# Performance work log

Hardware: AMD Instinct MI355X
Metric: run time of the kernel (lower is better)

## Reference

```python
import jax, jax.numpy as jnp
import numpy as np

N_NODES = 100000
N_EDGES = 800000


def setup_inputs() -> dict:
    key = jax.random.key(0)
    ks = jax.random.split(key, 9)
    def glorot(k, shape):
        lim = float(np.sqrt(6.0 / (shape[0] + shape[1])))
        return jax.random.uniform(k, shape, jnp.float32, -lim, lim)
    return {
        "x": jax.random.normal(ks[0], (N_NODES, 4), jnp.float32),
        "edge_index": jax.random.randint(ks[1], (2, N_EDGES), 0, N_NODES, jnp.int64),
        "edge_weight": jax.random.uniform(ks[2], (N_EDGES,), jnp.float32),
        "W1": glorot(ks[3], (4, 128)),
        "b1": jnp.zeros((128,), jnp.float32),
        "W2": glorot(ks[4], (128, 64)),
        "b2": jnp.zeros((64,), jnp.float32),
        "W3": glorot(ks[5], (64, 1)),
        "b3": jnp.zeros((1,), jnp.float32),
    }


def reference(x, edge_index, edge_weight, W1, b1, W2, b2, W3, b3):
    N = x.shape[0]
    # PyG GCNConv: add self loops (weight 1) and symmetric normalization.
    loop = jnp.arange(N)
    src = jnp.concatenate([edge_index[0], loop])  # [E+N]
    dst = jnp.concatenate([edge_index[1], loop])  # [E+N]
    w = jnp.concatenate([edge_weight, jnp.ones((N,), x.dtype)])
    deg = jax.ops.segment_sum(w, dst, num_segments=N)  # weighted in-degree
    dis = jnp.where(deg > 0, jax.lax.rsqrt(jnp.maximum(deg, 1e-12)), 0.0)
    norm = dis[src] * w * dis[dst]  # [E+N]

    def conv(h, W, b):
        h = h @ W                      # [N, F_out] transform first (F_out small)
        msg = norm[:, None] * h[src]   # gather + scale per edge
        return jax.ops.segment_sum(msg, dst, num_segments=N) + b

    h = jax.nn.relu(conv(x, W1, b1))
    h = jax.nn.relu(conv(h, W2, b2))
    return conv(h, W3, b3)
```

## Files before the change

### kernel.cpp

```cpp
#include <hip/hip_runtime.h>
#include <hip/hip_fp16.h>


constexpr int N = 100000;
constexpr int E = 800000;
constexpr int NBKT = 391;
constexpr int BCAP = 3072;
constexpr int GC = 125;
constexpr int CHUNK = 6400;

static inline int cdiv(int a, int b) { return (a + b - 1) / b; }

typedef __attribute__((ext_vector_type(8))) _Float16 f16x8;
typedef __attribute__((ext_vector_type(4))) float f32x4;

__global__ void k_zero(int* __restrict__ bucket_cursor) {
    int i = blockIdx.x * blockDim.x + threadIdx.x;
    if (i < NBKT) bucket_cursor[i] = 0;
}

__global__ __launch_bounds__(256) void k_coarse(const int* __restrict__ src,
                                                const int* __restrict__ dst,
                                                const float* __restrict__ w,
                                                int* __restrict__ bucket_cursor,
                                                int2* __restrict__ sorted) {
    __shared__ int hist[NBKT];
    __shared__ int base[NBKT];
    int t = threadIdx.x;
    for (int i = t; i < NBKT; i += 256) hist[i] = 0;
    __syncthreads();
    int begin = blockIdx.x * CHUNK;
    int ranks[25];
#pragma unroll
    for (int i = 0; i < 25; i++) {
        int e = begin + i * 256 + t;
        ranks[i] = atomicAdd(&hist[dst[e] >> 8], 1);
    }
    __syncthreads();
    for (int i = t; i < NBKT; i += 256) {
        int h = hist[i];
        base[i] = h ? atomicAdd(&bucket_cursor[i], h) : 0;
    }
    __syncthreads();
#pragma unroll
    for (int i = 0; i < 25; i++) {
        int e = begin + i * 256 + t;
        int d = dst[e], b = d >> 8;
        int pos = base[b] + ranks[i];
        if (pos < BCAP)
            sorted[(size_t)b * BCAP + pos] =
                make_int2(src[e] | ((d & 255) << 17), __float_as_int(w[e]));
    }
}

__global__ __launch_bounds__(256) void k_fine(const int2* __restrict__ sorted,
                                              const int* __restrict__ bucket_cursor,
                                              int cap, int2* __restrict__ payload,
                                              int* __restrict__ cursor,
                                              float* __restrict__ dis) {
    __shared__ int   ncnt[256];
    __shared__ float nwsum[256];
    int t = threadIdx.x, b = blockIdx.x;
    ncnt[t] = 0;
    nwsum[t] = 1.0f;
    __syncthreads();
    int cnt = bucket_cursor[b]; if (cnt > BCAP) cnt = BCAP;
    const int2* seg = sorted + (size_t)b * BCAP;
    for (int i = t; i < cnt; i += 256) {
        int2 r = seg[i];
        int s = r.x & 0x1FFFF, dlo = r.x >> 17;
        int pos = atomicAdd(&ncnt[dlo], 1);
        atomicAdd(&nwsum[dlo], __int_as_float(r.y));
        if (pos < cap)
            payload[(size_t)(b * 256 + dlo) * cap + pos] = make_int2(s, r.y);
    }
    __syncthreads();
    int n = b * 256 + t;
    if (n < N) {
        int c = ncnt[t]; if (c > cap) c = cap;
        cursor[n] = c;
        dis[n] = rsqrtf(nwsum[t]);
    }
}

__global__ void k_agg1(const float4* __restrict__ x, const float* __restrict__ dis,
                       const int* __restrict__ cursor, const int2* __restrict__ payload,
                       int cap, float4* __restrict__ agg1) {
    int n = blockIdx.x * blockDim.x + threadIdx.x;
    if (n >= N) return;
    float di = dis[n], sc = di * di;
    float4 v = x[n];
    float ax = sc * v.x, ay = sc * v.y, az = sc * v.z, aw = sc * v.w;
    int c = cursor[n];
    const int2* row = payload + (size_t)n * cap;
    for (int e = 0; e < c; e++) {
        int2 p = row[e];
        float nm = dis[p.x] * __int_as_float(p.y) * di;
        float4 u = x[p.x];
        ax = fmaf(nm, u.x, ax); ay = fmaf(nm, u.y, ay);
        az = fmaf(nm, u.z, az); aw = fmaf(nm, u.w, aw);
    }
    agg1[n] = make_float4(ax, ay, az, aw);
}

constexpr int HROW = 136;
__global__ __launch_bounds__(256) void k_fused_l1(const float4* __restrict__ agg1,
                                                  const float* __restrict__ W1,
                                                  const float* __restrict__ b1,
                                                  const float* __restrict__ W2,
                                                  __half* __restrict__ y2h) {
    __shared__ _Float16 h1lds[4][16 * HROW];
    int t = threadIdx.x, wave = t >> 6, lane = t & 63;
    int q = lane >> 4, c = lane & 15;
    _Float16* sh = h1lds[wave];

    int k1 = lane, k2 = lane + 64;
    float w10 = W1[0 * 128 + k1], w11 = W1[1 * 128 + k1];
    float w12 = W1[2 * 128 + k1], w13 = W1[3 * 128 + k1], bb1 = b1[k1];
    float w20 = W1[0 * 128 + k2], w21 = W1[1 * 128 + k2];
    float w22 = W1[2 * 128 + k2], w23 = W1[3 * 128 + k2], bb2 = b1[k2];

    f16x8 Bf[4][4];
#pragma unroll
    for (int kt = 0; kt < 4; kt++)
#pragma unroll
        for (int nt = 0; nt < 4; nt++)
#pragma unroll
            for (int j = 0; j < 8; j++)
                Bf[kt][nt][j] = (_Float16)W2[(kt * 32 + q * 8 + j) * 64 + nt * 16 + c];

    int wave_id = blockIdx.x * 4 + wave;
#pragma unroll
    for (int g = 0; g < 2; g++) {
        int n0 = (wave_id * 2 + g) * 16;
        if (n0 >= N) break;
#pragma unroll
        for (int m = 0; m < 16; m++) {
            float4 a = agg1[n0 + m];
            float v1 = bb1, v2 = bb2;
            v1 = fmaf(a.x, w10, v1); v1 = fmaf(a.y, w11, v1);
            v1 = fmaf(a.z, w12, v1); v1 = fmaf(a.w, w13, v1);
            v2 = fmaf(a.x, w20, v2); v2 = fmaf(a.y, w21, v2);
            v2 = fmaf(a.z, w22, v2); v2 = fmaf(a.w, w23, v2);
            sh[m * HROW + k1] = (_Float16)fmaxf(v1, 0.f);
            sh[m * HROW + k2] = (_Float16)fmaxf(v2, 0.f);
        }
        f32x4 C[4] = {{0.f, 0.f, 0.f, 0.f}, {0.f, 0.f, 0.f, 0.f},
                      {0.f, 0.f, 0.f, 0.f}, {0.f, 0.f, 0.f, 0.f}};
#pragma unroll
        for (int kt = 0; kt < 4; kt++) {
            f16x8 A = *(const f16x8*)&sh[c * HROW + kt * 32 + q * 8];
#pragma unroll
            for (int nt = 0; nt < 4; nt++)
                C[nt] = __builtin_amdgcn_mfma_f32_16x16x32_f16(A, Bf[kt][nt], C[nt], 0, 0, 0);
        }
#pragma unroll
        for (int nt = 0; nt < 4; nt++)
#pragma unroll
            for (int r = 0; r < 4; r++) {
                int node = n0 + q * 4 + r;
                y2h[(size_t)node * 64 + nt * 16 + c] = __float2half(C[nt][r]);
            }
    }
}

__global__ __launch_bounds__(256) void k_agg2_fused(
        const __half* __restrict__ y2h, const float* __restrict__ dis,
        const int* __restrict__ cursor, const int2* __restrict__ payload, int cap,
        const float* __restrict__ b2, const float* __restrict__ W3,
        const float* __restrict__ b3, float* __restrict__ s_out,
        float* __restrict__ out) {
    int t = threadIdx.x, wave = t >> 6, lane = t & 63;
    int n = blockIdx.x * 4 + wave;
    if (n >= N) return;
    float di = dis[n];
    float acc = di * di * __half2float(y2h[(size_t)n * 64 + lane]);
    int c = cursor[n];
    const int2* row = payload + (size_t)n * cap;
    int e = 0;
    for (; e + 3 < c; e += 4) {
        int2 p0 = row[e], p1 = row[e + 1], p2 = row[e + 2], p3 = row[e + 3];
        float v0 = __half2float(y2h[(size_t)p0.x * 64 + lane]);
        float v1 = __half2float(y2h[(size_t)p1.x * 64 + lane]);
        float v2 = __half2float(y2h[(size_t)p2.x * 64 + lane]);
        float v3 = __half2float(y2h[(size_t)p3.x * 64 + lane]);
        acc = fmaf(dis[p0.x] * __int_as_float(p0.y) * di, v0, acc);
        acc = fmaf(dis[p1.x] * __int_as_float(p1.y) * di, v1, acc);
        acc = fmaf(dis[p2.x] * __int_as_float(p2.y) * di, v2, acc);
        acc = fmaf(dis[p3.x] * __int_as_float(p3.y) * di, v3, acc);
    }
    for (; e < c; e++) {
        int2 p = row[e];
        acc = fmaf(dis[p.x] * __int_as_float(p.y) * di,
                   __half2float(y2h[(size_t)p.x * 64 + lane]), acc);
    }
    float h = fmaxf(acc + b2[lane], 0.f);
    float p = h * W3[lane];
#pragma unroll
    for (int off = 32; off > 0; off >>= 1) p += __shfl_down(p, off);
    if (lane == 0) {
        s_out[n] = p;
        out[n] = di * di * p + b3[0];
    }
}

__global__ void k_agg3(const float* __restrict__ s, const float* __restrict__ dis,
                       const int* __restrict__ cursor, const int2* __restrict__ payload,
                       int cap, float* __restrict__ out) {
    int n = blockIdx.x * blockDim.x + threadIdx.x;
    if (n >= N) return;
    float di = dis[n], acc = 0.f;
    int c = cursor[n];
    const int2* row = payload + (size_t)n * cap;
    for (int e = 0; e < c; e++) {
        int2 p = row[e];
        acc = fmaf(dis[p.x] * __int_as_float(p.y) * di, s[p.x], acc);
    }
    out[n] += acc;
}

extern "C" void kernel_launch(void* const* d_in, const int* in_sizes, int n_in,
                              void* d_out, int out_size, void* d_ws, size_t ws_size,
                              hipStream_t stream) {
    const float* x  = (const float*)d_in[0];
    const int*   ei = (const int*)d_in[1];
    const int* src = ei;
    const int* dst = ei + E;
    const float* w  = (const float*)d_in[2];
    const float* W1 = (const float*)d_in[3];
    const float* b1 = (const float*)d_in[4];
    const float* W2 = (const float*)d_in[5];
    const float* b2 = (const float*)d_in[6];
    const float* W3 = (const float*)d_in[7];
    const float* b3 = (const float*)d_in[8];
    float* out = (float*)d_out;

    int*    bcur    = (int*)d_ws;
    int*    cursor  = bcur + 512;
    float*  dis     = (float*)(cursor + N);
    float*  agg1    = dis + N;
    __half* y2h     = (__half*)(agg1 + 4 * N);
    float*  s       = agg1;
    int2*   sorted  = (int2*)((char*)y2h + (size_t)64 * N * sizeof(__half));
    int2*   payload = sorted + (size_t)NBKT * BCAP;
    size_t fixed_bytes = (size_t)(512 + 2 * N + 4 * N) * 4 + (size_t)64 * N * 2
                       + (size_t)NBKT * BCAP * 8;
    int cap = (int)((ws_size - fixed_bytes) / ((size_t)N * 8));
    if (cap > 64) cap = 64;

    k_zero       <<<cdiv(NBKT, 256), 256, 0, stream>>>(bcur);
    k_coarse     <<<GC,           256, 0, stream>>>(src, dst, w, bcur, sorted);
    k_fine       <<<NBKT,         256, 0, stream>>>(sorted, bcur, cap, payload, cursor, dis);
    k_agg1       <<<cdiv(N, 256), 256, 0, stream>>>((const float4*)x, dis, cursor, payload,
                                                    cap, (float4*)agg1);
    k_fused_l1   <<<cdiv(N / 16, 8), 256, 0, stream>>>((const float4*)agg1, W1, b1, W2, y2h);
    k_agg2_fused <<<cdiv(N, 4),   256, 0, stream>>>(y2h, dis, cursor, payload, cap,
                                                    b2, W3, b3, s, out);
    k_agg3       <<<cdiv(N, 256), 256, 0, stream>>>(s, dis, cursor, payload, cap, out);
}
```

Measured before the change: 198.6 us.

## Fold self-loops into CSR rows, cache edge norms, parallelize aggregation across lanes

The self-loop goes into slot 0 of each node's adjacency row, and rows are padded with zero entries to a multiple of 8 so the aggregation kernels can loop without a remainder. k_agg1 now splits each node over 16 lanes (4 edge slots by 4 features) and writes the computed per-edge norm back into the payload. k_agg2 and k_agg3 then read that cached norm instead of gathering dis again. k_agg2 processes 4 nodes per wave with 8-wide fp16 vector loads and two edge slots, and k_agg3 uses 8 lanes per node. The aim is more memory-level parallelism and fewer dependent gathers; the costs are extra padding writes and in-place mutation of the payload, and a row that fills cap may lose an edge to the self-loop slot.

```diff
diff --git a/kernel.cpp b/kernel.cpp
--- a/kernel.cpp
+++ b/kernel.cpp
@@ -61,7 +61,7 @@
     __shared__ int   ncnt[256];
     __shared__ float nwsum[256];
     int t = threadIdx.x, b = blockIdx.x;
-    ncnt[t] = 0;
+    ncnt[t] = 1;
     nwsum[t] = 1.0f;
     __syncthreads();
     int cnt = bucket_cursor[b]; if (cnt > BCAP) cnt = BCAP;
@@ -78,29 +78,39 @@
     int n = b * 256 + t;
     if (n < N) {
         int c = ncnt[t]; if (c > cap) c = cap;
+        int2* row = payload + (size_t)n * cap;
+        row[0] = make_int2(n, __float_as_int(1.0f));
+        int cpad = (c + 7) & ~7;
+        for (int e = c; e < cpad; e++) row[e] = make_int2(0, 0);
         cursor[n] = c;
         dis[n] = rsqrtf(nwsum[t]);
     }
 }
 
-__global__ void k_agg1(const float4* __restrict__ x, const float* __restrict__ dis,
-                       const int* __restrict__ cursor, const int2* __restrict__ payload,
-                       int cap, float4* __restrict__ agg1) {
-    int n = blockIdx.x * blockDim.x + threadIdx.x;
-    if (n >= N) return;
-    float di = dis[n], sc = di * di;
-    float4 v = x[n];
-    float ax = sc * v.x, ay = sc * v.y, az = sc * v.z, aw = sc * v.w;
-    int c = cursor[n];
-    const int2* row = payload + (size_t)n * cap;
-    for (int e = 0; e < c; e++) {
+__global__ __launch_bounds__(256) void k_agg1(const float* __restrict__ x,
+                                              const float* __restrict__ dis,
+                                              const int* __restrict__ cursor,
+                                              int2* __restrict__ payload, int cap,
+                                              float* __restrict__ agg1) {
+    int t = threadIdx.x, lane = t & 63, wave = t >> 6;
+    int nsub = lane >> 4, slot = (lane >> 2) & 3, feat = lane & 3;
+    int n = (blockIdx.x * 4 + wave) * 4 + nsub;
+    float di = dis[n];
+    int cnt = cursor[n];
+    int2* row = payload + (size_t)n * cap;
+    int iters = (cnt + 3) >> 2;
+    float acc = 0.f;
+    for (int it = 0; it < iters; it++) {
+        int e = it * 4 + slot;
         int2 p = row[e];
         float nm = dis[p.x] * __int_as_float(p.y) * di;
-        float4 u = x[p.x];
-        ax = fmaf(nm, u.x, ax); ay = fmaf(nm, u.y, ay);
-        az = fmaf(nm, u.z, az); aw = fmaf(nm, u.w, aw);
-    }
-    agg1[n] = make_float4(ax, ay, az, aw);
+        float xv = x[p.x * 4 + feat];
+        acc = fmaf(nm, xv, acc);
+        if (feat == 0) row[e].y = __float_as_int(nm);
+    }
+    acc += __shfl_xor(acc, 4);
+    acc += __shfl_xor(acc, 8);
+    if (slot == 0) agg1[n * 4 + feat] = acc;
 }
 
 constexpr int HROW = 136;
@@ -164,59 +174,64 @@
     }
 }
 
-__global__ __launch_bounds__(256) void k_agg2_fused(
-        const __half* __restrict__ y2h, const float* __restrict__ dis,
-        const int* __restrict__ cursor, const int2* __restrict__ payload, int cap,
-        const float* __restrict__ b2, const float* __restrict__ W3,
-        const float* __restrict__ b3, float* __restrict__ s_out,
-        float* __restrict__ out) {
-    int t = threadIdx.x, wave = t >> 6, lane = t & 63;
-    int n = blockIdx.x * 4 + wave;
-    if (n >= N) return;
-    float di = dis[n];
-    float acc = di * di * __half2float(y2h[(size_t)n * 64 + lane]);
-    int c = cursor[n];
+__global__ __launch_bounds__(256) void k_agg2(const __half* __restrict__ y2h,
+                                              const int* __restrict__ cursor,
+                                              const int2* __restrict__ payload, int cap,
+                                              const float* __restrict__ b2,
+                                              const float* __restrict__ W3,
+                                              float* __restrict__ s_out) {
+    int t = threadIdx.x, lane = t & 63, wave = t >> 6;
+    int nsub = lane >> 4, slot = (lane >> 3) & 1, k = lane & 7;
+    int n = (blockIdx.x * 4 + wave) * 4 + nsub;
+    float b2v[8], w3v[8];
+#pragma unroll
+    for (int j = 0; j < 8; j++) { b2v[j] = b2[k * 8 + j]; w3v[j] = W3[k * 8 + j]; }
+    int cnt = cursor[n];
     const int2* row = payload + (size_t)n * cap;
-    int e = 0;
-    for (; e + 3 < c; e += 4) {
-        int2 p0 = row[e], p1 = row[e + 1], p2 = row[e + 2], p3 = row[e + 3];
-        float v0 = __half2float(y2h[(size_t)p0.x * 64 + lane]);
-        float v1 = __half2float(y2h[(size_t)p1.x * 64 + lane]);
-        float v2 = __half2float(y2h[(size_t)p2.x * 64 + lane]);
-        float v3 = __half2float(y2h[(size_t)p3.x * 64 + lane]);
-        acc = fmaf(dis[p0.x] * __int_as_float(p0.y) * di, v0, acc);
-        acc = fmaf(dis[p1.x] * __int_as_float(p1.y) * di, v1, acc);
-        acc = fmaf(dis[p2.x] * __int_as_float(p2.y) * di, v2, acc);
-        acc = fmaf(dis[p3.x] * __int_as_float(p3.y) * di, v3, acc);
-    }
-    for (; e < c; e++) {
-        int2 p = row[e];
-        acc = fmaf(dis[p.x] * __int_as_float(p.y) * di,
-                   __half2float(y2h[(size_t)p.x * 64 + lane]), acc);
-    }
-    float h = fmaxf(acc + b2[lane], 0.f);
-    float p = h * W3[lane];
-#pragma unroll
-    for (int off = 32; off > 0; off >>= 1) p += __shfl_down(p, off);
-    if (lane == 0) {
-        s_out[n] = p;
-        out[n] = di * di * p + b3[0];
-    }
-}
-
-__global__ void k_agg3(const float* __restrict__ s, const float* __restrict__ dis,
-                       const int* __restrict__ cursor, const int2* __restrict__ payload,
-                       int cap, float* __restrict__ out) {
-    int n = blockIdx.x * blockDim.x + threadIdx.x;
-    if (n >= N) return;
-    float di = dis[n], acc = 0.f;
-    int c = cursor[n];
+    int iters = (cnt + 1) >> 1;
+    float acc[8] = {0.f, 0.f, 0.f, 0.f, 0.f, 0.f, 0.f, 0.f};
+    for (int it = 0; it < iters; it++) {
+        int2 p = row[it * 2 + slot];
+        float nm = __int_as_float(p.y);
+        f16x8 v = *(const f16x8*)(y2h + (size_t)p.x * 64 + k * 8);
+#pragma unroll
+        for (int j = 0; j < 8; j++)
+            acc[j] = fmaf(nm, (float)v[j], acc[j]);
+    }
+#pragma unroll
+    for (int j = 0; j < 8; j++) acc[j] += __shfl_xor(acc[j], 8);
+    float p_ = 0.f;
+#pragma unroll
+    for (int j = 0; j < 8; j++) {
+        float h = fmaxf(acc[j] + b2v[j], 0.f);
+        p_ = fmaf(h, w3v[j], p_);
+    }
+    p_ += __shfl_xor(p_, 1);
+    p_ += __shfl_xor(p_, 2);
+    p_ += __shfl_xor(p_, 4);
+    if (slot == 0 && k == 0) s_out[n] = p_;
+}
+
+__global__ __launch_bounds__(256) void k_agg3(const float* __restrict__ s,
+                                              const int* __restrict__ cursor,
+                                              const int2* __restrict__ payload, int cap,
+                                              const float* __restrict__ b3,
+                                              float* __restrict__ out) {
+    int t = threadIdx.x, lane = t & 63, wave = t >> 6;
+    int nsub = lane >> 3, slot = lane & 7;
+    int n = (blockIdx.x * 4 + wave) * 8 + nsub;
+    int cnt = cursor[n];
     const int2* row = payload + (size_t)n * cap;
-    for (int e = 0; e < c; e++) {
-        int2 p = row[e];
-        acc = fmaf(dis[p.x] * __int_as_float(p.y) * di, s[p.x], acc);
-    }
-    out[n] += acc;
+    int iters = (cnt + 7) >> 3;
+    float acc = 0.f;
+    for (int it = 0; it < iters; it++) {
+        int2 p = row[it * 8 + slot];
+        acc = fmaf(__int_as_float(p.y), s[p.x], acc);
+    }
+    acc += __shfl_xor(acc, 1);
+    acc += __shfl_xor(acc, 2);
+    acc += __shfl_xor(acc, 4);
+    if (slot == 0) out[n] = acc + b3[0];
 }
 
 extern "C" void kernel_launch(void* const* d_in, const int* in_sizes, int n_in,
@@ -248,13 +263,11 @@
     int cap = (int)((ws_size - fixed_bytes) / ((size_t)N * 8));
     if (cap > 64) cap = 64;
 
-    k_zero       <<<cdiv(NBKT, 256), 256, 0, stream>>>(bcur);
-    k_coarse     <<<GC,           256, 0, stream>>>(src, dst, w, bcur, sorted);
-    k_fine       <<<NBKT,         256, 0, stream>>>(sorted, bcur, cap, payload, cursor, dis);
-    k_agg1       <<<cdiv(N, 256), 256, 0, stream>>>((const float4*)x, dis, cursor, payload,
-                                                    cap, (float4*)agg1);
-    k_fused_l1   <<<cdiv(N / 16, 8), 256, 0, stream>>>((const float4*)agg1, W1, b1, W2, y2h);
-    k_agg2_fused <<<cdiv(N, 4),   256, 0, stream>>>(y2h, dis, cursor, payload, cap,
-                                                    b2, W3, b3, s, out);
-    k_agg3       <<<cdiv(N, 256), 256, 0, stream>>>(s, dis, cursor, payload, cap, out);
-}
+    k_zero    <<<cdiv(NBKT, 256), 256, 0, stream>>>(bcur);
+    k_coarse  <<<GC,              256, 0, stream>>>(src, dst, w, bcur, sorted);
+    k_fine    <<<NBKT,            256, 0, stream>>>(sorted, bcur, cap, payload, cursor, dis);
+    k_agg1    <<<N / 16,          256, 0, stream>>>(x, dis, cursor, payload, cap, agg1);
+    k_fused_l1<<<cdiv(N / 16, 8), 256, 0, stream>>>((const float4*)agg1, W1, b1, W2, y2h);
+    k_agg2    <<<N / 16,          256, 0, stream>>>(y2h, cursor, payload, cap, b2, W3, s);
+    k_agg3    <<<N / 32,          256, 0, stream>>>(s, cursor, payload, cap, b3, out);
+}
```

After: 169.9 us. 1.17x faster.
